# Optimization experiments

Hardware: AMD Instinct MI355X
Metric: run time of the kernel (lower is better)

The kernel has to match this reference:

```python
import jax, jax.numpy as jnp
import numpy as np

B, N, C = 16, 4096, 768
H = 12
D = C // H  # 64
SCALE = D ** -0.5


def setup_inputs() -> dict:
    key = jax.random.key(0)
    k1, k2, k3, k4 = jax.random.split(key, 4)
    x = jax.random.normal(k1, (B, N, C), dtype=jnp.float32)
    # packed qkv projection (bias=False): torch Linear(dim, 3*dim)
    w_qkv = jax.random.normal(k2, (C, 3 * C), dtype=jnp.float32) * 0.02
    # output projection Linear(dim, dim) with bias
    w_proj = jax.random.normal(k3, (C, C), dtype=jnp.float32) * 0.02
    b_proj = jax.random.normal(k4, (C,), dtype=jnp.float32) * 0.02
    return {"x": x, "w_qkv": w_qkv, "w_proj": w_proj, "b_proj": b_proj}


def reference(x, w_qkv, w_proj, b_proj):
    b, n, c = x.shape
    # packed qkv: [B,N,3C] -> [3,B,H,N,D]
    qkv = (x @ w_qkv).reshape(b, n, 3, H, D).transpose(2, 0, 3, 1, 4)
    q, k, v = qkv[0], qkv[1], qkv[2]  # each [B,H,N,D]
    # kernelized (linear) attention: kv = (k^T v) * scale  -> [B,H,D,D]
    kv = jnp.einsum("bhnd,bhne->bhde", k, v) * SCALE
    # out = gelu(q) @ gelu(kv)  (exact/erf gelu, matching torch F.gelu default)
    gq = jax.nn.gelu(q, approximate=False)
    gkv = jax.nn.gelu(kv, approximate=False)
    out = jnp.einsum("bhtd,bhde->bhte", gq, gkv)  # [B,H,N,D]
    out = out.transpose(0, 2, 1, 3).reshape(b, n, c)  # b t (h d)
    return out @ w_proj + b_proj
```

## Files before the change

kernel.cpp:

```cpp
#include <hip/hip_runtime.h>
#include <hip/hip_bf16.h>


typedef __attribute__((ext_vector_type(8))) short short8_t;
typedef __attribute__((ext_vector_type(4))) float f32x4_t;

typedef __attribute__((address_space(1))) void as1_void;
typedef __attribute__((address_space(3))) void as3_void;

__device__ __forceinline__ void gload_lds16(const void* g, void* l) {
    __builtin_amdgcn_global_load_lds(
        (as1_void*)(unsigned long long)(g),
        (as3_void*)(unsigned long long)(l), 16, 0, 0);
}

__device__ __forceinline__ float gelu_f(float x) {
    float x2 = x * x;
    float t = x * fmaf(0.0356774081f, x2, 0.7978845608f);
    float e = __expf(2.0f * t);
    float th = 1.0f - 2.0f / (e + 1.0f);
    return 0.5f * x * (1.0f + th);
}

__device__ __forceinline__ unsigned short to_bf16(float f) {
    __hip_bfloat16 h = __float2bfloat16(f);
    return *reinterpret_cast<unsigned short*>(&h);
}

__device__ __forceinline__ f32x4_t mfma16(short8_t a, short8_t b, f32x4_t c) {
    return __builtin_amdgcn_mfma_f32_16x16x32_bf16(a, b, c, 0, 0, 0);
}

__global__ __launch_bounds__(256) void k_cvt_bf16(const float* __restrict__ in,
                                                  unsigned short* __restrict__ out,
                                                  long n) {
    long i = (long)blockIdx.x * blockDim.x + threadIdx.x;
    long stride = (long)gridDim.x * blockDim.x;
    for (long idx = i * 4; idx < n; idx += stride * 4) {
        float4 v = *(const float4*)(in + idx);
        ushort4 o;
        o.x = to_bf16(v.x); o.y = to_bf16(v.y); o.z = to_bf16(v.z); o.w = to_bf16(v.w);
        *(ushort4*)(out + idx) = o;
    }
}

__global__ __launch_bounds__(256) void k_wprep(const float* __restrict__ w_qkv,
                                               const float* __restrict__ w_proj,
                                               unsigned short* __restrict__ wqkvT,
                                               unsigned short* __restrict__ wpT,
                                               unsigned short* __restrict__ wqkv_bf) {
    const int blk = blockIdx.x, tid = threadIdx.x;
    if (blk < 864) {
        int gid = blk * 256 + tid;
        int c = gid / 96, r0 = (gid % 96) * 8;
        short8_t o;
#pragma unroll
        for (int i = 0; i < 8; ++i)
            o[i] = (short)to_bf16(w_qkv[(size_t)(r0 + i) * 2304 + c]);
        *(short8_t*)(wqkvT + (size_t)c * 768 + r0) = o;
    } else if (blk < 1152) {
        int gid = (blk - 864) * 256 + tid;
        int c = gid / 96, r0 = (gid % 96) * 8;
        short8_t o;
#pragma unroll
        for (int i = 0; i < 8; ++i)
            o[i] = (short)to_bf16(w_proj[(size_t)(r0 + i) * 768 + c]);
        *(short8_t*)(wpT + (size_t)c * 768 + r0) = o;
    } else {
        long i = (long)(blk - 1152) * 256 + tid;
        long stride = 432L * 256;
        for (long idx = i * 4; idx < 1769472L; idx += stride * 4) {
            float4 v = *(const float4*)(w_qkv + idx);
            ushort4 o;
            o.x = to_bf16(v.x); o.y = to_bf16(v.y); o.z = to_bf16(v.z); o.w = to_bf16(v.w);
            *(ushort4*)(wqkv_bf + idx) = o;
        }
    }
}

template<bool GELU_EPI, bool BATCHED_B, bool BF16_OUT, bool BIAS>
__global__ __launch_bounds__(512, 2)
void k_gemm256(const unsigned short* __restrict__ A, int lda,
               const unsigned short* __restrict__ Bt, int ldb,
               void* __restrict__ Cout, int ldc,
               const float* __restrict__ bias,
               int tiles_n, int K) {
    __shared__ __attribute__((aligned(16))) unsigned short lds[2][2][2][128 * 64];

    const int nwg = gridDim.x;
    int bid = blockIdx.x;
    bid = (bid & 7) * (nwg >> 3) + (bid >> 3);

    const int tn = bid % tiles_n, tm = bid / tiles_n;
    const int row0 = tm * 256, col0 = tn * 256;

    const unsigned short* Bb = Bt;
    if (BATCHED_B) Bb += (size_t)(row0 >> 12) * 768 * 768;

    const int tid = threadIdx.x;
    const int lane = tid & 63;
    const int w = tid >> 6;
    const int wm = w >> 2;
    const int wn = w & 3;
    const int lr = lane & 15, lg = lane >> 4;

    const int c0 = tid, c1 = 512 + tid;
    const int sr0 = c0 >> 3, sk0 = (c0 & 7) ^ (sr0 & 7);
    const int sr1 = c1 >> 3, sk1 = (c1 & 7) ^ (sr1 & 7);

    auto stageA = [&](int buf, int half, int kt) {
        const unsigned short* base = A + (size_t)(row0 + half * 128) * lda + kt * 64;
        gload_lds16(base + (size_t)sr0 * lda + sk0 * 8, &lds[0][buf][half][c0 * 8]);
        gload_lds16(base + (size_t)sr1 * lda + sk1 * 8, &lds[0][buf][half][c1 * 8]);
    };
    auto stageB = [&](int buf, int half, int kt) {
        const unsigned short* base = Bb + (size_t)(col0 + half * 128) * ldb + kt * 64;
        gload_lds16(base + (size_t)sr0 * ldb + sk0 * 8, &lds[1][buf][half][c0 * 8]);
        gload_lds16(base + (size_t)sr1 * ldb + sk1 * 8, &lds[1][buf][half][c1 * 8]);
    };
    auto ldA = [&](int buf, int mi, int ks) -> short8_t {
        int row = mi * 16 + lr;
        int kc = (ks * 4 + lg) ^ (row & 7);
        return *(const short8_t*)&lds[0][buf][wm][row * 64 + kc * 8];
    };
    auto ldB = [&](int buf, int nj, int ks) -> short8_t {
        int row = wn * 64 + nj * 16 + lr;
        int half = row >> 7, rl = row & 127;
        int kc = (ks * 4 + lg) ^ (rl & 7);
        return *(const short8_t*)&lds[1][buf][half][rl * 64 + kc * 8];
    };

    f32x4_t acc[8][4] = {};
    short8_t bfrag[4][2];
    short8_t afrP[2][4];

#define FENCE asm volatile("" ::: "memory")
#define MFMACL(r0i, par)                                                        \
    __builtin_amdgcn_s_setprio(1);                                              \
    _Pragma("unroll") for (int nj = 0; nj < 4; ++nj) {                          \
        acc[r0i][nj]     = mfma16(afrP[par][0], bfrag[nj][0], acc[r0i][nj]);    \
        acc[r0i][nj]     = mfma16(afrP[par][1], bfrag[nj][1], acc[r0i][nj]);    \
        acc[r0i + 1][nj] = mfma16(afrP[par][2], bfrag[nj][0], acc[r0i + 1][nj]);\
        acc[r0i + 1][nj] = mfma16(afrP[par][3], bfrag[nj][1], acc[r0i + 1][nj]);\
    }                                                                           \
    __builtin_amdgcn_s_setprio(0);

#define GROUP(cb, nb, tnx)                                                      \
    { afrP[0][0] = ldA(cb, 0, 0); afrP[0][1] = ldA(cb, 0, 1);                   \
      afrP[0][2] = ldA(cb, 1, 0); afrP[0][3] = ldA(cb, 1, 1);                   \
      afrP[1][0] = ldA(cb, 2, 0); afrP[1][1] = ldA(cb, 2, 1);                   \
      afrP[1][2] = ldA(cb, 3, 0); afrP[1][3] = ldA(cb, 3, 1);                   \
      asm volatile("s_waitcnt lgkmcnt(4)" ::: "memory");                        \
      __builtin_amdgcn_sched_barrier(0);                                        \
      MFMACL(0, 0)                                                              \
      stageB(cb, 0, tnx);                                                       \
      FENCE; __builtin_amdgcn_s_barrier(); FENCE;                               \
      afrP[0][0] = ldA(cb, 4, 0); afrP[0][1] = ldA(cb, 4, 1);                   \
      afrP[0][2] = ldA(cb, 5, 0); afrP[0][3] = ldA(cb, 5, 1);                   \
      asm volatile("s_waitcnt lgkmcnt(4)" ::: "memory");                        \
      __builtin_amdgcn_sched_barrier(0);                                        \
      MFMACL(2, 1)                                                              \
      stageB(cb, 1, tnx);                                                       \
      FENCE; __builtin_amdgcn_s_barrier(); FENCE;                               \
      afrP[1][0] = ldA(cb, 6, 0); afrP[1][1] = ldA(cb, 6, 1);                   \
      afrP[1][2] = ldA(cb, 7, 0); afrP[1][3] = ldA(cb, 7, 1);                   \
      asm volatile("s_waitcnt lgkmcnt(4)" ::: "memory");                        \
      __builtin_amdgcn_sched_barrier(0);                                        \
      MFMACL(4, 0)                                                              \
      asm volatile("s_waitcnt vmcnt(8)" ::: "memory");                          \
      FENCE; __builtin_amdgcn_s_barrier(); FENCE;                               \
      asm volatile("s_waitcnt lgkmcnt(0)" ::: "memory");                        \
      __builtin_amdgcn_sched_barrier(0);                                        \
      MFMACL(6, 1)                                                              \
      _Pragma("unroll") for (int nj = 0; nj < 4; ++nj)                          \
          _Pragma("unroll") for (int ks = 0; ks < 2; ++ks)                      \
              bfrag[nj][ks] = ldB(nb, nj, ks);                                  \
      stageA(cb, 0, tnx); stageA(cb, 1, tnx);                                   \
      asm volatile("s_waitcnt vmcnt(8)" ::: "memory");                          \
      FENCE; __builtin_amdgcn_s_barrier(); FENCE;                               \
    }

    const int nt = K >> 6;
    const int niter = nt >> 1;

    stageA(0, 0, 0); stageA(0, 1, 0); stageB(0, 0, 0); stageB(0, 1, 0);
    asm volatile("s_waitcnt vmcnt(0)" ::: "memory");
    __builtin_amdgcn_s_barrier();
    FENCE;
    stageB(1, 0, 1); stageB(1, 1, 1); stageA(1, 0, 1); stageA(1, 1, 1);
#pragma unroll
    for (int nj = 0; nj < 4; ++nj)
#pragma unroll
        for (int ks = 0; ks < 2; ++ks)
            bfrag[nj][ks] = ldB(0, nj, ks);
    asm volatile("s_waitcnt lgkmcnt(0)" ::: "memory");
    FENCE;

    for (int it = 0; it < niter; ++it) {
        const int tA = (2 * it + 2 < nt) ? 2 * it + 2 : 0;
        const int tB = (2 * it + 3 < nt) ? 2 * it + 3 : 0;
        GROUP(0, 1, tA);
        GROUP(1, 0, tB);
    }
    asm volatile("s_waitcnt vmcnt(0)" ::: "memory");
#undef GROUP
#undef MFMACL
#undef FENCE

    const int rbase = row0 + wm * 128 + (lg << 2);
    const int cbase = col0 + wn * 64 + lr;
#pragma unroll
    for (int mi = 0; mi < 8; ++mi)
#pragma unroll
        for (int nj = 0; nj < 4; ++nj)
#pragma unroll
            for (int r = 0; r < 4; ++r) {
                int row = rbase + mi * 16 + r;
                int col = cbase + nj * 16;
                float v = acc[mi][nj][r];
                if (GELU_EPI) v = gelu_f(v);
                if (BIAS) v += bias[col];
                if (BF16_OUT)
                    ((unsigned short*)Cout)[(size_t)row * ldc + col] = to_bf16(v);
                else
                    ((float*)Cout)[(size_t)row * ldc + col] = v;
            }
}

__global__ __launch_bounds__(256)
void k_gemm128(const unsigned short* __restrict__ A, int lda,
               const unsigned short* __restrict__ Bt, int ldb,
               unsigned short* __restrict__ C, int ldc,
               int tiles_n, int K) {
    __shared__ __attribute__((aligned(16))) unsigned short As[128 * 64];
    __shared__ __attribute__((aligned(16))) unsigned short Bs[128 * 64];

    const int nwg = gridDim.x;
    int bid = blockIdx.x;
    bid = (bid & 7) * (nwg >> 3) + (bid >> 3);

    const int tn = bid % tiles_n, tm = bid / tiles_n;
    const int row0 = tm * 128, col0 = tn * 128;

    const int tid = threadIdx.x, lane = tid & 63, w = tid >> 6;
    const int wm = w >> 1, wn = w & 1;
    const int lr = lane & 15, lg = lane >> 4;

    f32x4_t acc[4][4] = {};

    const int nt = K >> 6;
    for (int kt = 0; kt < nt; ++kt) {
#pragma unroll
        for (int i = 0; i < 4; ++i) {
            int ch = i * 256 + tid;
            int sr = ch >> 3, sk = (ch & 7) ^ (sr & 7);
            gload_lds16(A + (size_t)(row0 + sr) * lda + kt * 64 + sk * 8, As + ch * 8);
            gload_lds16(Bt + (size_t)(col0 + sr) * ldb + kt * 64 + sk * 8, Bs + ch * 8);
        }
        __syncthreads();
#pragma unroll
        for (int ks = 0; ks < 2; ++ks) {
            short8_t a[4], b[4];
#pragma unroll
            for (int mi = 0; mi < 4; ++mi) {
                int row = wm * 64 + mi * 16 + lr;
                a[mi] = *(const short8_t*)(As + row * 64 + (((ks * 4 + lg) ^ (row & 7)) << 3));
            }
#pragma unroll
            for (int nj = 0; nj < 4; ++nj) {
                int row = wn * 64 + nj * 16 + lr;
                b[nj] = *(const short8_t*)(Bs + row * 64 + (((ks * 4 + lg) ^ (row & 7)) << 3));
            }
#pragma unroll
            for (int mi = 0; mi < 4; ++mi)
#pragma unroll
                for (int nj = 0; nj < 4; ++nj)
                    acc[mi][nj] = mfma16(a[mi], b[nj], acc[mi][nj]);
        }
        __syncthreads();
    }

    const int rbase = row0 + wm * 64 + (lg << 2);
    const int cbase = col0 + wn * 64 + lr;
#pragma unroll
    for (int mi = 0; mi < 4; ++mi)
#pragma unroll
        for (int nj = 0; nj < 4; ++nj)
#pragma unroll
            for (int r = 0; r < 4; ++r)
                C[(size_t)(rbase + mi * 16 + r) * ldc + cbase + nj * 16] = to_bf16(acc[mi][nj][r]);
}

__global__ __launch_bounds__(256) void k_G(const unsigned short* __restrict__ xb,
                                           unsigned short* __restrict__ Gst) {
    static const signed char TI[21] = {0,0,0,0,0,0,1,1,1,1,1,2,2,2,2,3,3,3,4,4,5};
    static const signed char TJ[21] = {0,1,2,3,4,5,1,2,3,4,5,2,3,4,5,3,4,5,4,5,5};
    int bid = blockIdx.x;
    bid = (bid & 7) * 42 + (bid >> 3);
    const int b = bid / 21, t = bid % 21;
    const int d0 = TI[t] * 128, e0 = TJ[t] * 128;
    const bool diag = (d0 == e0);
    const unsigned short* xB = xb + (size_t)b * 4096 * 768;

    __shared__ __attribute__((aligned(16))) unsigned short lds[2][2][128 * 64];

    const int tid = threadIdx.x, lane = tid & 63, w = tid >> 6;
    const int colg = tid & 15;
    const int rq8 = (tid >> 4) & 7;
    const int blk = tid >> 7;
    const int wm = w >> 1, wn = w & 1;
    const int lr = lane & 15, lg = lane >> 4;
    const int base0 = (blk ? e0 : d0) + colg * 8;
    const int tb = diag ? 0 : 1;
    const bool active = (!diag) || (blk == 0);

    f32x4_t acc[4][4] = {};
    short8_t ra[8];

    auto loadx = [&](int it) {
        if (!active) return;
        const size_t rbase = (size_t)(it * 64 + rq8 * 8) * 768 + base0;
#pragma unroll
        for (int rr = 0; rr < 8; ++rr)
            ra[rr] = *(const short8_t*)(xB + rbase + (size_t)rr * 768);
    };
    auto writes = [&](int buf) {
        if (!active) return;
#pragma unroll
        for (int j = 0; j < 8; ++j) {
            const int c = colg * 8 + j;
            const int sw3 = ((c & 7) ^ (c >> 3)) & 7;
            short8_t v;
#pragma unroll
            for (int rr = 0; rr < 8; ++rr) v[rr] = ra[rr][j];
            *(short8_t*)(&lds[buf][blk][c * 64 + ((rq8 ^ sw3) << 3)]) = v;
        }
    };
    auto ldfrag = [&](int buf, int tile, int cbase, int o) -> short8_t {
        const int c = cbase + lr;
        const int sw3 = ((c & 7) ^ (c >> 3)) & 7;
        return *(const short8_t*)(&lds[buf][tile][c * 64 + ((o ^ sw3) << 3)]);
    };

    loadx(0);
    writes(0);
    __syncthreads();

    for (int it = 0; it < 64; ++it) {
        const int buf = it & 1;
        if (it < 63) loadx(it + 1);
#pragma unroll
        for (int ks = 0; ks < 2; ++ks) {
            short8_t af[4], bf[4];
#pragma unroll
            for (int mi = 0; mi < 4; ++mi)
                af[mi] = ldfrag(buf, 0, wm * 64 + mi * 16, ks * 4 + lg);
#pragma unroll
            for (int nj = 0; nj < 4; ++nj)
                bf[nj] = ldfrag(buf, tb, wn * 64 + nj * 16, ks * 4 + lg);
#pragma unroll
            for (int mi = 0; mi < 4; ++mi)
#pragma unroll
                for (int nj = 0; nj < 4; ++nj)
                    acc[mi][nj] = mfma16(af[mi], bf[nj], acc[mi][nj]);
        }
        if (it < 63) writes(buf ^ 1);
        __syncthreads();
    }

    const int dbase = d0 + wm * 64 + (lg << 2);
    const int ebase = e0 + wn * 64 + lr;
#pragma unroll
    for (int mi = 0; mi < 4; ++mi)
#pragma unroll
        for (int nj = 0; nj < 4; ++nj)
#pragma unroll
            for (int r = 0; r < 4; ++r)
                Gst[((size_t)b * 768 + dbase + mi * 16 + r) * 768 + ebase + nj * 16] =
                    to_bf16(acc[mi][nj][r]);

    if (!diag) {
        unsigned short* T = &lds[0][0][0];
#pragma unroll
        for (int mi = 0; mi < 4; ++mi)
#pragma unroll
            for (int nj = 0; nj < 4; ++nj) {
                const int el = wn * 64 + nj * 16 + lr;
                const int sig = ((el ^ (el >> 3)) & 7) << 1;
                const int s = wm * 16 + mi * 4 + lg;
                uint2 pk;
                pk.x = (unsigned int)to_bf16(acc[mi][nj][0]) |
                       ((unsigned int)to_bf16(acc[mi][nj][1]) << 16);
                pk.y = (unsigned int)to_bf16(acc[mi][nj][2]) |
                       ((unsigned int)to_bf16(acc[mi][nj][3]) << 16);
                *(uint2*)(&T[el * 128 + ((s ^ sig) << 2)]) = pk;
            }
        __syncthreads();
#pragma unroll
        for (int i = 0; i < 8; ++i) {
            const int el = i * 16 + (tid >> 4);
            const int p = tid & 15;
            const int sig = ((el ^ (el >> 3)) & 7) << 1;
            short8_t v = *(const short8_t*)(&T[el * 128 + (((2 * p) ^ sig) << 2)]);
            *(short8_t*)(Gst + ((size_t)b * 768 + e0 + el) * 768 + d0 + p * 8) = v;
        }
    }
}

__global__ __launch_bounds__(256) void k_kvM(const unsigned short* __restrict__ wqkv_bf,
                                             const unsigned short* __restrict__ Tst,
                                             const unsigned short* __restrict__ wpT,
                                             unsigned short* __restrict__ MT) {
    const int bh = blockIdx.x;
    const int b = bh / 12, h = bh % 12;
    const unsigned short* kptr = wqkv_bf + 768 + h * 64;
    const unsigned short* vptr = Tst + (size_t)b * 768 * 768 + h * 64;

    __shared__ __attribute__((aligned(16))) unsigned short kT[64 * 64];
    __shared__ __attribute__((aligned(16))) unsigned short vT[64 * 64];
    __shared__ __attribute__((aligned(16))) unsigned short As[64 * 64];
    __shared__ __attribute__((aligned(16))) unsigned short Bs[256 * 64];

    const int tid = threadIdx.x, lane = tid & 63, w = tid >> 6;
    const int np = tid >> 3;
    const int g = tid & 7;
    const int lr = lane & 15, lg = lane >> 4;

    f32x4_t acc[4] = {};

    for (int it = 0; it < 12; ++it) {
        const size_t r = (size_t)(it * 64 + 2 * np);
        short8_t k0 = *(const short8_t*)(kptr + r * 2304 + g * 8);
        short8_t k1 = *(const short8_t*)(kptr + (r + 1) * 2304 + g * 8);
        short8_t v0 = *(const short8_t*)(vptr + r * 768 + g * 8);
        short8_t v1 = *(const short8_t*)(vptr + (r + 1) * 768 + g * 8);
        __syncthreads();
#pragma unroll
        for (int j = 0; j < 8; ++j) {
            const int d = g * 8 + j;
            const int e = d * 64 + ((2 * np) ^ (((d ^ (d >> 3)) & 7) << 3));
            *(unsigned int*)(kT + e) =
                (unsigned int)(unsigned short)k0[j] | ((unsigned int)(unsigned short)k1[j] << 16);
            *(unsigned int*)(vT + e) =
                (unsigned int)(unsigned short)v0[j] | ((unsigned int)(unsigned short)v1[j] << 16);
        }
        __syncthreads();
#pragma unroll
        for (int ks = 0; ks < 2; ++ks) {
            const int d = w * 16 + lr;
            short8_t a = *(const short8_t*)(kT + d * 64 +
                (((ks * 4 + lg) ^ ((d ^ (d >> 3)) & 7)) << 3));
#pragma unroll
            for (int nj = 0; nj < 4; ++nj) {
                const int e2 = nj * 16 + lr;
                short8_t bf = *(const short8_t*)(vT + e2 * 64 +
                    (((ks * 4 + lg) ^ ((e2 ^ (e2 >> 3)) & 7)) << 3));
                acc[nj] = __builtin_amdgcn_mfma_f32_16x16x32_bf16(a, bf, acc[nj], 0, 0, 0);
            }
        }
    }

    {
        const int drow = w * 16 + (lg << 2);
#pragma unroll
        for (int nj = 0; nj < 4; ++nj)
#pragma unroll
            for (int r = 0; r < 4; ++r) {
                const int d = drow + r;
                const int e = nj * 16 + lr;
                As[d * 64 + ((((e >> 3) ^ (d & 7)) << 3) | (e & 7))] =
                    to_bf16(gelu_f(acc[nj][r] * 0.125f));
            }
    }

    for (int ct = 0; ct < 3; ++ct) {
        const int c0 = ct * 256;
        short8_t rb[8];
#pragma unroll
        for (int i = 0; i < 8; ++i) {
            int ch = i * 256 + tid, row = ch >> 3, kc = ch & 7;
            rb[i] = *(const short8_t*)(wpT + (size_t)(c0 + row) * 768 + h * 64 + kc * 8);
        }
        __syncthreads();
#pragma unroll
        for (int i = 0; i < 8; ++i) {
            int ch = i * 256 + tid, row = ch >> 3, kc = ch & 7;
            *(short8_t*)(Bs + row * 64 + ((kc ^ (row & 7)) * 8)) = rb[i];
        }
        __syncthreads();

        f32x4_t acc2[4][4] = {};
#pragma unroll
        for (int ks = 0; ks < 2; ++ks) {
            short8_t a[4], bfr[4];
#pragma unroll
            for (int mi = 0; mi < 4; ++mi) {
                int row = mi * 16 + lr;
                a[mi] = *(const short8_t*)(As + row * 64 + (((ks * 4 + lg) ^ (row & 7)) * 8));
            }
#pragma unroll
            for (int nj = 0; nj < 4; ++nj) {
                int row = w * 64 + nj * 16 + lr;
                bfr[nj] = *(const short8_t*)(Bs + row * 64 + (((ks * 4 + lg) ^ (row & 7)) * 8));
            }
#pragma unroll
            for (int mi = 0; mi < 4; ++mi)
#pragma unroll
                for (int nj = 0; nj < 4; ++nj)
                    acc2[mi][nj] = __builtin_amdgcn_mfma_f32_16x16x32_bf16(a[mi], bfr[nj], acc2[mi][nj], 0, 0, 0);
        }
        __syncthreads();

#pragma unroll
        for (int mi = 0; mi < 4; ++mi)
#pragma unroll
            for (int nj = 0; nj < 4; ++nj) {
                unsigned int w0 = (unsigned int)to_bf16(acc2[mi][nj][0]) |
                                  ((unsigned int)to_bf16(acc2[mi][nj][1]) << 16);
                unsigned int w1 = (unsigned int)to_bf16(acc2[mi][nj][2]) |
                                  ((unsigned int)to_bf16(acc2[mi][nj][3]) << 16);
                uint2 pk; pk.x = w0; pk.y = w1;
                *(uint2*)(Bs + (w * 64 + nj * 16 + lr) * 64 + mi * 16 + lg * 4) = pk;
            }
        __syncthreads();
#pragma unroll
        for (int i = 0; i < 8; ++i) {
            int ch = i * 256 + tid, cl = ch >> 3, dk = ch & 7;
            short8_t v = *(const short8_t*)(Bs + cl * 64 + dk * 8);
            *(short8_t*)(MT + ((size_t)(b * 768) + c0 + cl) * 768 + h * 64 + dk * 8) = v;
        }
    }
}

extern "C" void kernel_launch(void* const* d_in, const int* in_sizes, int n_in,
                              void* d_out, int out_size, void* d_ws, size_t ws_size,
                              hipStream_t stream) {
    const float* x      = (const float*)d_in[0];
    const float* w_qkv  = (const float*)d_in[1];
    const float* w_proj = (const float*)d_in[2];
    const float* b_proj = (const float*)d_in[3];
    float* out = (float*)d_out;
    char* ws = (char*)d_ws;

    unsigned short* q_gelu  = (unsigned short*)(ws);
    unsigned short* wqkvT   = (unsigned short*)(ws + 100663296);
    unsigned short* wqkv_bf = (unsigned short*)(ws + 104202240);
    unsigned short* G_bf    = (unsigned short*)(ws + 107741184);
    unsigned short* T_bf    = (unsigned short*)(ws + 126615552);
    unsigned short* MT      = (unsigned short*)(ws + 145489920);
    unsigned short* xb   = (unsigned short*)d_out;
    unsigned short* wpT  = (unsigned short*)((char*)d_out + 136314880);

    k_cvt_bf16<<<2048, 256, 0, stream>>>(x, xb, 50331648L);
    k_wprep<<<1584, 256, 0, stream>>>(w_qkv, w_proj, wqkvT, wpT, wqkv_bf);
    k_gemm256<true, false, true, false><<<768, 512, 0, stream>>>(
        xb, 768, wqkvT, 768, q_gelu, 768, nullptr, 3, 768);
    k_G<<<336, 256, 0, stream>>>(xb, G_bf);
    k_gemm128<<<576, 256, 0, stream>>>(
        G_bf, 768, wqkvT + (size_t)1536 * 768, 768, T_bf, 768, 6, 768);
    k_kvM<<<192, 256, 0, stream>>>(wqkv_bf, T_bf, wpT, MT);
    k_gemm256<false, true, false, true><<<768, 512, 0, stream>>>(
        q_gelu, 768, MT, 768, out, 768, b_proj, 3, 768);
}
```

Baseline: 386.1 us.

## Replace pipelined 256x256 GEMM with simple 128x128 single-buffered GEMM template

Removes the hand-scheduled 256x256-tile, double-buffered, 512-thread GEMM and generalizes the simple 128x128 single-buffered kernel into a template with the GELU, batched-B, bias and output-format epilogues. The two large GEMMs now launch four times as many smaller workgroups, and the T GEMM reuses the same template. This simplifies the code and raises occupancy and workgroup count, but drops the software pipelining and halves per-tile operand reuse, so global and LDS traffic per FLOP go up and load latency is no longer hidden.

```diff
diff --git a/kernel.cpp b/kernel.cpp
--- a/kernel.cpp
+++ b/kernel.cpp
@@ -79,138 +79,67 @@
 }
 
 template<bool GELU_EPI, bool BATCHED_B, bool BF16_OUT, bool BIAS>
-__global__ __launch_bounds__(512, 2)
-void k_gemm256(const unsigned short* __restrict__ A, int lda,
+__global__ __launch_bounds__(256)
+void k_gemm128(const unsigned short* __restrict__ A, int lda,
                const unsigned short* __restrict__ Bt, int ldb,
                void* __restrict__ Cout, int ldc,
                const float* __restrict__ bias,
                int tiles_n, int K) {
-    __shared__ __attribute__((aligned(16))) unsigned short lds[2][2][2][128 * 64];
+    __shared__ __attribute__((aligned(16))) unsigned short As[128 * 64];
+    __shared__ __attribute__((aligned(16))) unsigned short Bs[128 * 64];
 
     const int nwg = gridDim.x;
     int bid = blockIdx.x;
     bid = (bid & 7) * (nwg >> 3) + (bid >> 3);
 
     const int tn = bid % tiles_n, tm = bid / tiles_n;
-    const int row0 = tm * 256, col0 = tn * 256;
+    const int row0 = tm * 128, col0 = tn * 128;
 
     const unsigned short* Bb = Bt;
     if (BATCHED_B) Bb += (size_t)(row0 >> 12) * 768 * 768;
 
-    const int tid = threadIdx.x;
-    const int lane = tid & 63;
-    const int w = tid >> 6;
-    const int wm = w >> 2;
-    const int wn = w & 3;
+    const int tid = threadIdx.x, lane = tid & 63, w = tid >> 6;
+    const int wm = w >> 1, wn = w & 1;
     const int lr = lane & 15, lg = lane >> 4;
 
-    const int c0 = tid, c1 = 512 + tid;
-    const int sr0 = c0 >> 3, sk0 = (c0 & 7) ^ (sr0 & 7);
-    const int sr1 = c1 >> 3, sk1 = (c1 & 7) ^ (sr1 & 7);
-
-    auto stageA = [&](int buf, int half, int kt) {
-        const unsigned short* base = A + (size_t)(row0 + half * 128) * lda + kt * 64;
-        gload_lds16(base + (size_t)sr0 * lda + sk0 * 8, &lds[0][buf][half][c0 * 8]);
-        gload_lds16(base + (size_t)sr1 * lda + sk1 * 8, &lds[0][buf][half][c1 * 8]);
-    };
-    auto stageB = [&](int buf, int half, int kt) {
-        const unsigned short* base = Bb + (size_t)(col0 + half * 128) * ldb + kt * 64;
-        gload_lds16(base + (size_t)sr0 * ldb + sk0 * 8, &lds[1][buf][half][c0 * 8]);
-        gload_lds16(base + (size_t)sr1 * ldb + sk1 * 8, &lds[1][buf][half][c1 * 8]);
-    };
-    auto ldA = [&](int buf, int mi, int ks) -> short8_t {
-        int row = mi * 16 + lr;
-        int kc = (ks * 4 + lg) ^ (row & 7);
-        return *(const short8_t*)&lds[0][buf][wm][row * 64 + kc * 8];
-    };
-    auto ldB = [&](int buf, int nj, int ks) -> short8_t {
-        int row = wn * 64 + nj * 16 + lr;
-        int half = row >> 7, rl = row & 127;
-        int kc = (ks * 4 + lg) ^ (rl & 7);
-        return *(const short8_t*)&lds[1][buf][half][rl * 64 + kc * 8];
-    };
-
-    f32x4_t acc[8][4] = {};
-    short8_t bfrag[4][2];
-    short8_t afrP[2][4];
-
-#define FENCE asm volatile("" ::: "memory")
-#define MFMACL(r0i, par)                                                        \
-    __builtin_amdgcn_s_setprio(1);                                              \
-    _Pragma("unroll") for (int nj = 0; nj < 4; ++nj) {                          \
-        acc[r0i][nj]     = mfma16(afrP[par][0], bfrag[nj][0], acc[r0i][nj]);    \
-        acc[r0i][nj]     = mfma16(afrP[par][1], bfrag[nj][1], acc[r0i][nj]);    \
-        acc[r0i + 1][nj] = mfma16(afrP[par][2], bfrag[nj][0], acc[r0i + 1][nj]);\
-        acc[r0i + 1][nj] = mfma16(afrP[par][3], bfrag[nj][1], acc[r0i + 1][nj]);\
-    }                                                                           \
-    __builtin_amdgcn_s_setprio(0);
-
-#define GROUP(cb, nb, tnx)                                                      \
-    { afrP[0][0] = ldA(cb, 0, 0); afrP[0][1] = ldA(cb, 0, 1);                   \
-      afrP[0][2] = ldA(cb, 1, 0); afrP[0][3] = ldA(cb, 1, 1);                   \
-      afrP[1][0] = ldA(cb, 2, 0); afrP[1][1] = ldA(cb, 2, 1);                   \
-      afrP[1][2] = ldA(cb, 3, 0); afrP[1][3] = ldA(cb, 3, 1);                   \
-      asm volatile("s_waitcnt lgkmcnt(4)" ::: "memory");                        \
-      __builtin_amdgcn_sched_barrier(0);                                        \
-      MFMACL(0, 0)                                                              \
-      stageB(cb, 0, tnx);                                                       \
-      FENCE; __builtin_amdgcn_s_barrier(); FENCE;                               \
-      afrP[0][0] = ldA(cb, 4, 0); afrP[0][1] = ldA(cb, 4, 1);                   \
-      afrP[0][2] = ldA(cb, 5, 0); afrP[0][3] = ldA(cb, 5, 1);                   \
-      asm volatile("s_waitcnt lgkmcnt(4)" ::: "memory");                        \
-      __builtin_amdgcn_sched_barrier(0);                                        \
-      MFMACL(2, 1)                                                              \
-      stageB(cb, 1, tnx);                                                       \
-      FENCE; __builtin_amdgcn_s_barrier(); FENCE;                               \
-      afrP[1][0] = ldA(cb, 6, 0); afrP[1][1] = ldA(cb, 6, 1);                   \
-      afrP[1][2] = ldA(cb, 7, 0); afrP[1][3] = ldA(cb, 7, 1);                   \
-      asm volatile("s_waitcnt lgkmcnt(4)" ::: "memory");                        \
-      __builtin_amdgcn_sched_barrier(0);                                        \
-      MFMACL(4, 0)                                                              \
-      asm volatile("s_waitcnt vmcnt(8)" ::: "memory");                          \
-      FENCE; __builtin_amdgcn_s_barrier(); FENCE;                               \
-      asm volatile("s_waitcnt lgkmcnt(0)" ::: "memory");                        \
-      __builtin_amdgcn_sched_barrier(0);                                        \
-      MFMACL(6, 1)                                                              \
-      _Pragma("unroll") for (int nj = 0; nj < 4; ++nj)                          \
-          _Pragma("unroll") for (int ks = 0; ks < 2; ++ks)                      \
-              bfrag[nj][ks] = ldB(nb, nj, ks);                                  \
-      stageA(cb, 0, tnx); stageA(cb, 1, tnx);                                   \
-      asm volatile("s_waitcnt vmcnt(8)" ::: "memory");                          \
-      FENCE; __builtin_amdgcn_s_barrier(); FENCE;                               \
-    }
+    f32x4_t acc[4][4] = {};
 
     const int nt = K >> 6;
-    const int niter = nt >> 1;
-
-    stageA(0, 0, 0); stageA(0, 1, 0); stageB(0, 0, 0); stageB(0, 1, 0);
-    asm volatile("s_waitcnt vmcnt(0)" ::: "memory");
-    __builtin_amdgcn_s_barrier();
-    FENCE;
-    stageB(1, 0, 1); stageB(1, 1, 1); stageA(1, 0, 1); stageA(1, 1, 1);
-#pragma unroll
-    for (int nj = 0; nj < 4; ++nj)
-#pragma unroll
-        for (int ks = 0; ks < 2; ++ks)
-            bfrag[nj][ks] = ldB(0, nj, ks);
-    asm volatile("s_waitcnt lgkmcnt(0)" ::: "memory");
-    FENCE;
-
-    for (int it = 0; it < niter; ++it) {
-        const int tA = (2 * it + 2 < nt) ? 2 * it + 2 : 0;
-        const int tB = (2 * it + 3 < nt) ? 2 * it + 3 : 0;
-        GROUP(0, 1, tA);
-        GROUP(1, 0, tB);
-    }
-    asm volatile("s_waitcnt vmcnt(0)" ::: "memory");
-#undef GROUP
-#undef MFMACL
-#undef FENCE
-
-    const int rbase = row0 + wm * 128 + (lg << 2);
+    for (int kt = 0; kt < nt; ++kt) {
+#pragma unroll
+        for (int i = 0; i < 4; ++i) {
+            int ch = i * 256 + tid;
+            int sr = ch >> 3, sk = (ch & 7) ^ (sr & 7);
+            gload_lds16(A + (size_t)(row0 + sr) * lda + kt * 64 + sk * 8, As + ch * 8);
+            gload_lds16(Bb + (size_t)(col0 + sr) * ldb + kt * 64 + sk * 8, Bs + ch * 8);
+        }
+        __syncthreads();
+#pragma unroll
+        for (int ks = 0; ks < 2; ++ks) {
+            short8_t a[4], b[4];
+#pragma unroll
+            for (int mi = 0; mi < 4; ++mi) {
+                int row = wm * 64 + mi * 16 + lr;
+                a[mi] = *(const short8_t*)(As + row * 64 + (((ks * 4 + lg) ^ (row & 7)) << 3));
+            }
+#pragma unroll
+            for (int nj = 0; nj < 4; ++nj) {
+                int row = wn * 64 + nj * 16 + lr;
+                b[nj] = *(const short8_t*)(Bs + row * 64 + (((ks * 4 + lg) ^ (row & 7)) << 3));
+            }
+#pragma unroll
+            for (int mi = 0; mi < 4; ++mi)
+#pragma unroll
+                for (int nj = 0; nj < 4; ++nj)
+                    acc[mi][nj] = mfma16(a[mi], b[nj], acc[mi][nj]);
+        }
+        __syncthreads();
+    }
+
+    const int rbase = row0 + wm * 64 + (lg << 2);
     const int cbase = col0 + wn * 64 + lr;
 #pragma unroll
-    for (int mi = 0; mi < 8; ++mi)
+    for (int mi = 0; mi < 4; ++mi)
 #pragma unroll
         for (int nj = 0; nj < 4; ++nj)
 #pragma unroll
@@ -227,70 +156,6 @@
             }
 }
 
-__global__ __launch_bounds__(256)
-void k_gemm128(const unsigned short* __restrict__ A, int lda,
-               const unsigned short* __restrict__ Bt, int ldb,
-               unsigned short* __restrict__ C, int ldc,
-               int tiles_n, int K) {
-    __shared__ __attribute__((aligned(16))) unsigned short As[128 * 64];
-    __shared__ __attribute__((aligned(16))) unsigned short Bs[128 * 64];
-
-    const int nwg = gridDim.x;
-    int bid = blockIdx.x;
-    bid = (bid & 7) * (nwg >> 3) + (bid >> 3);
-
-    const int tn = bid % tiles_n, tm = bid / tiles_n;
-    const int row0 = tm * 128, col0 = tn * 128;
-
-    const int tid = threadIdx.x, lane = tid & 63, w = tid >> 6;
-    const int wm = w >> 1, wn = w & 1;
-    const int lr = lane & 15, lg = lane >> 4;
-
-    f32x4_t acc[4][4] = {};
-
-    const int nt = K >> 6;
-    for (int kt = 0; kt < nt; ++kt) {
-#pragma unroll
-        for (int i = 0; i < 4; ++i) {
-            int ch = i * 256 + tid;
-            int sr = ch >> 3, sk = (ch & 7) ^ (sr & 7);
-            gload_lds16(A + (size_t)(row0 + sr) * lda + kt * 64 + sk * 8, As + ch * 8);
-            gload_lds16(Bt + (size_t)(col0 + sr) * ldb + kt * 64 + sk * 8, Bs + ch * 8);
-        }
-        __syncthreads();
-#pragma unroll
-        for (int ks = 0; ks < 2; ++ks) {
-            short8_t a[4], b[4];
-#pragma unroll
-            for (int mi = 0; mi < 4; ++mi) {
-                int row = wm * 64 + mi * 16 + lr;
-                a[mi] = *(const short8_t*)(As + row * 64 + (((ks * 4 + lg) ^ (row & 7)) << 3));
-            }
-#pragma unroll
-            for (int nj = 0; nj < 4; ++nj) {
-                int row = wn * 64 + nj * 16 + lr;
-                b[nj] = *(const short8_t*)(Bs + row * 64 + (((ks * 4 + lg) ^ (row & 7)) << 3));
-            }
-#pragma unroll
-            for (int mi = 0; mi < 4; ++mi)
-#pragma unroll
-                for (int nj = 0; nj < 4; ++nj)
-                    acc[mi][nj] = mfma16(a[mi], b[nj], acc[mi][nj]);
-        }
-        __syncthreads();
-    }
-
-    const int rbase = row0 + wm * 64 + (lg << 2);
-    const int cbase = col0 + wn * 64 + lr;
-#pragma unroll
-    for (int mi = 0; mi < 4; ++mi)
-#pragma unroll
-        for (int nj = 0; nj < 4; ++nj)
-#pragma unroll
-            for (int r = 0; r < 4; ++r)
-                C[(size_t)(rbase + mi * 16 + r) * ldc + cbase + nj * 16] = to_bf16(acc[mi][nj][r]);
-}
-
 __global__ __launch_bounds__(256) void k_G(const unsigned short* __restrict__ xb,
                                            unsigned short* __restrict__ Gst) {
     static const signed char TI[21] = {0,0,0,0,0,0,1,1,1,1,1,2,2,2,2,3,3,3,4,4,5};
@@ -553,12 +418,12 @@
 
     k_cvt_bf16<<<2048, 256, 0, stream>>>(x, xb, 50331648L);
     k_wprep<<<1584, 256, 0, stream>>>(w_qkv, w_proj, wqkvT, wpT, wqkv_bf);
-    k_gemm256<true, false, true, false><<<768, 512, 0, stream>>>(
-        xb, 768, wqkvT, 768, q_gelu, 768, nullptr, 3, 768);
+    k_gemm128<true, false, true, false><<<3072, 256, 0, stream>>>(
+        xb, 768, wqkvT, 768, q_gelu, 768, nullptr, 6, 768);
     k_G<<<336, 256, 0, stream>>>(xb, G_bf);
-    k_gemm128<<<576, 256, 0, stream>>>(
-        G_bf, 768, wqkvT + (size_t)1536 * 768, 768, T_bf, 768, 6, 768);
+    k_gemm128<false, false, true, false><<<576, 256, 0, stream>>>(
+        G_bf, 768, wqkvT + (size_t)1536 * 768, 768, T_bf, 768, nullptr, 6, 768);
     k_kvM<<<192, 256, 0, stream>>>(wqkv_bf, T_bf, wpT, MT);
-    k_gemm256<false, true, false, true><<<768, 512, 0, stream>>>(
-        q_gelu, 768, MT, 768, out, 768, b_proj, 3, 768);
-}
+    k_gemm128<false, true, false, true><<<3072, 256, 0, stream>>>(
+        q_gelu, 768, MT, 768, out, 768, b_proj, 6, 768);
+}
```

Result: slower. 441.2 us (+14.3%).
